# Kernel tuning notes

Measured on AMD Instinct MI355X. Metric: run time of the kernel, lower is better.

Reference implementation:

```python
import jax, jax.numpy as jnp
import numpy as np

N, F, D, K, H, O = 100000, 128, 16, 8, 256, 256  # nodes, feat, degree, num_hash, hash_dim, out_dim


def setup_inputs() -> dict:
    key = jax.random.key(0)
    k1, k2, k3, k4, k5 = jax.random.split(key, 5)
    x = jax.random.normal(k1, (N, F), dtype=jnp.float32)
    nbr_idx = jax.random.randint(k2, (N, D), 0, N, dtype=jnp.int32)
    # fixed sign hash matrices, one per hasher: {+1,-1}^{F x H}
    R = (jax.random.uniform(k3, (K, F, H)) > 0.5).astype(jnp.float32) * 2.0 - 1.0
    lim = float(np.sqrt(6.0 / (K * H + O)))  # xavier_uniform for Linear(K*H, O)
    Ws = jax.random.uniform(k4, (O, K * H), jnp.float32, -lim, lim)
    Wn = jax.random.uniform(k5, (O, K * H), jnp.float32, -lim, lim)
    bias = jnp.zeros((O,), dtype=jnp.float32)
    return {"x": x, "nbr_idx": nbr_idx, "R": R, "Ws": Ws, "Wn": Wn, "bias": bias}


def reference(x, nbr_idx, R, Ws, Wn, bias):
    n, f = x.shape
    k, _, h = R.shape
    # gather neighbor feats [N, D, F] and degree-mean -> [N, F]
    # (hashing is linear, so mean(hash(neigh)) == hash(mean(neigh)))
    neigh_mean = jnp.mean(x[nbr_idx], axis=1)
    # hash with all K hashers and concatenate streams: [N, K*H]
    hashed_neigh = jnp.einsum('nf,kfh->nkh', neigh_mean, R).reshape(n, k * h)
    hashed_self = jnp.einsum('nf,kfh->nkh', x, R).reshape(n, k * h)
    out = hashed_neigh @ Wn.T + hashed_self @ Ws.T + bias
    return jax.nn.elu(out)
```

## Files before the change

kernel.cpp:

```cpp
#include <hip/hip_runtime.h>
#include <hip/hip_bf16.h>
#include <math.h>

#define NN 100000
#define FF 128
#define DD 16
#define KK 8
#define HH 256
#define OO 256
#define KH 2048

using frag_t  = __attribute__((ext_vector_type(8))) short;
using f32x4   = __attribute__((ext_vector_type(4))) float;
using ushort8 = __attribute__((ext_vector_type(8))) unsigned short;

static __device__ __forceinline__ float bf2f(unsigned int u16) {
    union { unsigned int i; float f; } v; v.i = u16 << 16; return v.f;
}
static __device__ __forceinline__ unsigned short f2bf(float f) {
    union { float f; unsigned int i; } v; v.f = f;
    unsigned int x = v.i;
    x += 0x7fffu + ((x >> 16) & 1u);
    return (unsigned short)(x >> 16);
}

__global__ __launch_bounds__(256) void k_cast(const float* __restrict__ x,
                                              unsigned short* __restrict__ xb) {
    int t = blockIdx.x * 256 + threadIdx.x;
    const float4* xv = (const float4*)x;
    float4 a = xv[2 * t], b = xv[2 * t + 1];
    ushort8 o;
    o[0] = f2bf(a.x); o[1] = f2bf(a.y); o[2] = f2bf(a.z); o[3] = f2bf(a.w);
    o[4] = f2bf(b.x); o[5] = f2bf(b.y); o[6] = f2bf(b.z); o[7] = f2bf(b.w);
    *(ushort8*)(xb + (size_t)t * 8) = o;
}

__global__ __launch_bounds__(256) void k_wgemm(const float* __restrict__ R,
                                               const float* __restrict__ Ws,
                                               const float* __restrict__ Wn,
                                               float* __restrict__ P) {
    __shared__ float a_s[16][68];
    __shared__ float w_s[16][68];
    int bx = blockIdx.x, by = blockIdx.y, bz = blockIdx.z;
    const float* W = (bx < 2) ? Wn : Ws;
    int fbase = (bx & 1) * 64;
    int t = threadIdx.x;
    int tx = t & 15, ty = t >> 4;
    int lf = t >> 2;
    int j4 = (t & 3) * 4;
    float acc[4][4] = {};
    const float* Rb = R + (size_t)bz * (FF * HH) + (size_t)(fbase + lf) * HH;
    const float* Wb = W + (size_t)(by * 64 + lf) * KH + (size_t)bz * 256;
    for (int ks = 0; ks < 16; ++ks) {
        float4 av = *(const float4*)(Rb + ks * 16 + j4);
        float4 wv = *(const float4*)(Wb + ks * 16 + j4);
        __syncthreads();
        a_s[j4 + 0][lf] = av.x; a_s[j4 + 1][lf] = av.y;
        a_s[j4 + 2][lf] = av.z; a_s[j4 + 3][lf] = av.w;
        w_s[j4 + 0][lf] = wv.x; w_s[j4 + 1][lf] = wv.y;
        w_s[j4 + 2][lf] = wv.z; w_s[j4 + 3][lf] = wv.w;
        __syncthreads();
#pragma unroll
        for (int jj = 0; jj < 16; ++jj) {
            float ar[4], wr[4];
#pragma unroll
            for (int i = 0; i < 4; ++i) ar[i] = a_s[jj][ty * 4 + i];
#pragma unroll
            for (int j = 0; j < 4; ++j) wr[j] = w_s[jj][tx * 4 + j];
#pragma unroll
            for (int i = 0; i < 4; ++i)
#pragma unroll
                for (int j = 0; j < 4; ++j) acc[i][j] += ar[i] * wr[j];
        }
    }
    float* Pb = P + (size_t)bz * 65536 + (size_t)(bx * 64) * 256 + by * 64;
#pragma unroll
    for (int i = 0; i < 4; ++i) {
        float4 v = make_float4(acc[i][0], acc[i][1], acc[i][2], acc[i][3]);
        *(float4*)(Pb + (size_t)(ty * 4 + i) * 256 + tx * 4) = v;
    }
}

__global__ __launch_bounds__(256) void k_comb(const float* __restrict__ P,
                                              unsigned short* __restrict__ Bbf) {
    __shared__ float tsh[64][65];
    int bf = blockIdx.x, bo = blockIdx.y;
    int t = threadIdx.x;
    for (int e = t; e < 4096; e += 256) {
        int r = e >> 6, c = e & 63;
        float s = 0.f;
#pragma unroll
        for (int z = 0; z < 8; ++z)
            s += P[(size_t)z * 65536 + (size_t)(bf * 64 + r) * 256 + bo * 64 + c];
        tsh[r][c] = s;
    }
    __syncthreads();
    for (int e = t; e < 4096; e += 256) {
        int r = e >> 6, c = e & 63;
        Bbf[(size_t)(bo * 64 + r) * 256 + bf * 64 + c] = f2bf(tsh[c][r]);
    }
}

__global__ __launch_bounds__(512, 4) void k_fused(const unsigned short* __restrict__ xb,
                                                  const int* __restrict__ nbr,
                                                  const unsigned short* __restrict__ Bw,
                                                  const float* __restrict__ bias,
                                                  float* __restrict__ C) {
    __shared__ unsigned short Als[64][264];
    __shared__ unsigned short Bls[256][72];
    int m0 = blockIdx.x * 64;
    int t = threadIdx.x;
    int lane = t & 63, wv = t >> 6;
    int l15 = lane & 15, quad = lane >> 4;

    ushort8 bst[4];
    int brow[4], bcol[4];
#pragma unroll
    for (int s = 0; s < 4; ++s) {
        int c = s * 512 + t;
        brow[s] = c >> 3; bcol[s] = (c & 7) * 8;
        bst[s] = *(const ushort8*)(Bw + (size_t)brow[s] * 256 + bcol[s]);
    }

    const int rbase = wv * 8;
#pragma unroll 2
    for (int r = 0; r < 8; ++r) {
        int row = rbase + r;
        int node = m0 + row; if (node >= NN) node = NN - 1;
        node = __builtin_amdgcn_readfirstlane(node);
        const int* nb = nbr + (size_t)node * 16;
        unsigned int self = *(const unsigned int*)(xb + (size_t)node * 128 + lane * 2);
        float s0 = 0.f, s1 = 0.f;
#pragma unroll
        for (int d = 0; d < 16; ++d) {
            int idx = nb[d];
            unsigned int v = *(const unsigned int*)(xb + (size_t)idx * 128 + lane * 2);
            s0 += bf2f(v & 0xffffu);
            s1 += bf2f(v >> 16);
        }
        s0 *= 0.0625f; s1 *= 0.0625f;
        *(unsigned int*)&Als[row][lane * 2] =
            (unsigned int)f2bf(s0) | ((unsigned int)f2bf(s1) << 16);
        *(unsigned int*)&Als[row][128 + lane * 2] = self;
    }
#pragma unroll
    for (int s = 0; s < 4; ++s) *(ushort8*)&Bls[brow[s]][bcol[s]] = bst[s];
    __syncthreads();

    f32x4 acc[4][2] = {};
#pragma unroll 1
    for (int kt = 0; kt < 4; ++kt) {
        if (kt < 3) {
#pragma unroll
            for (int s = 0; s < 4; ++s)
                bst[s] = *(const ushort8*)(Bw + (size_t)brow[s] * 256 + (kt + 1) * 64 + bcol[s]);
        }
#pragma unroll
        for (int k2 = 0; k2 < 2; ++k2) {
            frag_t af[4], bfr[2];
#pragma unroll
            for (int i = 0; i < 4; ++i)
                af[i] = *(const frag_t*)&Als[i * 16 + l15][kt * 64 + k2 * 32 + quad * 8];
#pragma unroll
            for (int j = 0; j < 2; ++j)
                bfr[j] = *(const frag_t*)&Bls[wv * 32 + j * 16 + l15][k2 * 32 + quad * 8];
#pragma unroll
            for (int i = 0; i < 4; ++i)
#pragma unroll
                for (int j = 0; j < 2; ++j)
                    acc[i][j] = __builtin_amdgcn_mfma_f32_16x16x32_bf16(af[i], bfr[j], acc[i][j], 0, 0, 0);
        }
        __syncthreads();
        if (kt < 3) {
#pragma unroll
            for (int s = 0; s < 4; ++s) *(ushort8*)&Bls[brow[s]][bcol[s]] = bst[s];
            __syncthreads();
        }
    }
#pragma unroll
    for (int j = 0; j < 2; ++j) {
        int col = wv * 32 + j * 16 + l15;
        float bv = bias[col];
#pragma unroll
        for (int i = 0; i < 4; ++i) {
            int row0 = m0 + i * 16 + quad * 4;
#pragma unroll
            for (int r = 0; r < 4; ++r) {
                int row = row0 + r;
                if (row < NN) {
                    float v = acc[i][j][r] + bv;
                    C[(size_t)row * 256 + col] = (v > 0.f) ? v : expm1f(v);
                }
            }
        }
    }
}

extern "C" void kernel_launch(void* const* d_in, const int* in_sizes, int n_in,
                              void* d_out, int out_size, void* d_ws, size_t ws_size,
                              hipStream_t stream) {
    const float* x    = (const float*)d_in[0];
    const int*   nbr  = (const int*)d_in[1];
    const float* R    = (const float*)d_in[2];
    const float* Ws   = (const float*)d_in[3];
    const float* Wn   = (const float*)d_in[4];
    const float* bias = (const float*)d_in[5];
    float* out = (float*)d_out;

    char* ws = (char*)d_ws;
    unsigned short* xb  = (unsigned short*)(ws);
    float*          P   = (float*)(ws + 25600000);
    unsigned short* Bbf = (unsigned short*)(ws + 25600000 + 2097152);

    hipLaunchKernelGGL(k_cast,   dim3(6250),    dim3(256), 0, stream, x, xb);
    hipLaunchKernelGGL(k_wgemm,  dim3(4, 4, 8), dim3(256), 0, stream, R, Ws, Wn, P);
    hipLaunchKernelGGL(k_comb,   dim3(4, 4),    dim3(256), 0, stream, P, Bbf);
    hipLaunchKernelGGL(k_fused,  dim3(1563),    dim3(512), 0, stream, xb, nbr, Bbf, bias, out);
}
```

Measured before the change: 270.2 us.

## Widen neighbor gather, read B fragments from global, stage output stores

```diff
diff --git a/kernel.cpp b/kernel.cpp
--- a/kernel.cpp
+++ b/kernel.cpp
@@ -16,6 +16,12 @@
 
 static __device__ __forceinline__ float bf2f(unsigned int u16) {
     union { unsigned int i; float f; } v; v.i = u16 << 16; return v.f;
+}
+static __device__ __forceinline__ float blo(unsigned int u) {
+    union { unsigned int i; float f; } v; v.i = u << 16; return v.f;
+}
+static __device__ __forceinline__ float bhi(unsigned int u) {
+    union { unsigned int i; float f; } v; v.i = u & 0xffff0000u; return v.f;
 }
 static __device__ __forceinline__ unsigned short f2bf(float f) {
     union { float f; unsigned int i; } v; v.f = f;
@@ -106,92 +112,99 @@
                                                   const unsigned short* __restrict__ Bw,
                                                   const float* __restrict__ bias,
                                                   float* __restrict__ C) {
-    __shared__ unsigned short Als[64][264];
-    __shared__ unsigned short Bls[256][72];
+    __shared__ __align__(16) char smraw[64 * 264 * 2];
+    unsigned short (*Als)[264] = (unsigned short (*)[264])smraw;
+    float* Fls = (float*)smraw;
+    const int FLS_W = 260;
+
     int m0 = blockIdx.x * 64;
     int t = threadIdx.x;
     int lane = t & 63, wv = t >> 6;
     int l15 = lane & 15, quad = lane >> 4;
-
-    ushort8 bst[4];
-    int brow[4], bcol[4];
-#pragma unroll
-    for (int s = 0; s < 4; ++s) {
-        int c = s * 512 + t;
-        brow[s] = c >> 3; bcol[s] = (c & 7) * 8;
-        bst[s] = *(const ushort8*)(Bw + (size_t)brow[s] * 256 + bcol[s]);
-    }
-
-    const int rbase = wv * 8;
-#pragma unroll 2
-    for (int r = 0; r < 8; ++r) {
-        int row = rbase + r;
+    int l16 = lane & 15, r4 = lane >> 4;
+    int selbase = (lane & 48) << 2;
+
+#pragma unroll
+    for (int g = 0; g < 2; ++g) {
+        int row = wv * 8 + g * 4 + r4;
         int node = m0 + row; if (node >= NN) node = NN - 1;
-        node = __builtin_amdgcn_readfirstlane(node);
-        const int* nb = nbr + (size_t)node * 16;
-        unsigned int self = *(const unsigned int*)(xb + (size_t)node * 128 + lane * 2);
-        float s0 = 0.f, s1 = 0.f;
-#pragma unroll
-        for (int d = 0; d < 16; ++d) {
-            int idx = nb[d];
-            unsigned int v = *(const unsigned int*)(xb + (size_t)idx * 128 + lane * 2);
-            s0 += bf2f(v & 0xffffu);
-            s1 += bf2f(v >> 16);
-        }
-        s0 *= 0.0625f; s1 *= 0.0625f;
-        *(unsigned int*)&Als[row][lane * 2] =
-            (unsigned int)f2bf(s0) | ((unsigned int)f2bf(s1) << 16);
-        *(unsigned int*)&Als[row][128 + lane * 2] = self;
-    }
-#pragma unroll
-    for (int s = 0; s < 4; ++s) *(ushort8*)&Bls[brow[s]][bcol[s]] = bst[s];
+        int myidx = nbr[(size_t)node * 16 + l16];
+        uint4 selfv = *(const uint4*)(xb + (size_t)node * 128 + l16 * 8);
+        float s[8] = {0.f, 0.f, 0.f, 0.f, 0.f, 0.f, 0.f, 0.f};
+#pragma unroll
+        for (int h = 0; h < 2; ++h) {
+            uint4 gv[8];
+#pragma unroll
+            for (int d = 0; d < 8; ++d) {
+                int bi = __builtin_amdgcn_ds_bpermute(selbase + ((h * 8 + d) << 2), myidx);
+                gv[d] = *(const uint4*)(xb + (size_t)bi * 128 + l16 * 8);
+            }
+#pragma unroll
+            for (int d = 0; d < 8; ++d) {
+                s[0] += blo(gv[d].x); s[1] += bhi(gv[d].x);
+                s[2] += blo(gv[d].y); s[3] += bhi(gv[d].y);
+                s[4] += blo(gv[d].z); s[5] += bhi(gv[d].z);
+                s[6] += blo(gv[d].w); s[7] += bhi(gv[d].w);
+            }
+        }
+        ushort8 o;
+#pragma unroll
+        for (int k = 0; k < 8; ++k) o[k] = f2bf(s[k] * 0.0625f);
+        *(ushort8*)&Als[row][l16 * 8] = o;
+        *(uint4*)&Als[row][128 + l16 * 8] = selfv;
+    }
     __syncthreads();
 
     f32x4 acc[4][2] = {};
 #pragma unroll 1
     for (int kt = 0; kt < 4; ++kt) {
-        if (kt < 3) {
-#pragma unroll
-            for (int s = 0; s < 4; ++s)
-                bst[s] = *(const ushort8*)(Bw + (size_t)brow[s] * 256 + (kt + 1) * 64 + bcol[s]);
-        }
 #pragma unroll
         for (int k2 = 0; k2 < 2; ++k2) {
-            frag_t af[4], bfr[2];
+            frag_t bfr[2], af[4];
+#pragma unroll
+            for (int j = 0; j < 2; ++j)
+                bfr[j] = *(const frag_t*)(Bw + (size_t)(wv * 32 + j * 16 + l15) * 256
+                                             + kt * 64 + k2 * 32 + quad * 8);
 #pragma unroll
             for (int i = 0; i < 4; ++i)
                 af[i] = *(const frag_t*)&Als[i * 16 + l15][kt * 64 + k2 * 32 + quad * 8];
 #pragma unroll
-            for (int j = 0; j < 2; ++j)
-                bfr[j] = *(const frag_t*)&Bls[wv * 32 + j * 16 + l15][k2 * 32 + quad * 8];
-#pragma unroll
             for (int i = 0; i < 4; ++i)
 #pragma unroll
                 for (int j = 0; j < 2; ++j)
                     acc[i][j] = __builtin_amdgcn_mfma_f32_16x16x32_bf16(af[i], bfr[j], acc[i][j], 0, 0, 0);
         }
-        __syncthreads();
-        if (kt < 3) {
-#pragma unroll
-            for (int s = 0; s < 4; ++s) *(ushort8*)&Bls[brow[s]][bcol[s]] = bst[s];
-            __syncthreads();
-        }
-    }
-#pragma unroll
-    for (int j = 0; j < 2; ++j) {
-        int col = wv * 32 + j * 16 + l15;
-        float bv = bias[col];
-#pragma unroll
-        for (int i = 0; i < 4; ++i) {
-            int row0 = m0 + i * 16 + quad * 4;
-#pragma unroll
-            for (int r = 0; r < 4; ++r) {
-                int row = row0 + r;
-                if (row < NN) {
-                    float v = acc[i][j][r] + bv;
-                    C[(size_t)row * 256 + col] = (v > 0.f) ? v : expm1f(v);
+    }
+
+    float bv[2];
+#pragma unroll
+    for (int j = 0; j < 2; ++j) bv[j] = bias[wv * 32 + j * 16 + l15];
+#pragma unroll
+    for (int p = 0; p < 2; ++p) {
+        __syncthreads();
+#pragma unroll
+        for (int ii = 0; ii < 2; ++ii) {
+            int i = p * 2 + ii;
+#pragma unroll
+            for (int j = 0; j < 2; ++j) {
+                int col = wv * 32 + j * 16 + l15;
+#pragma unroll
+                for (int r = 0; r < 4; ++r) {
+                    int lr = ii * 16 + quad * 4 + r;
+                    float v = acc[i][j][r] + bv[j];
+                    v = (v > 0.f) ? v : expm1f(v);
+                    Fls[lr * FLS_W + col] = v;
                 }
             }
+        }
+        __syncthreads();
+#pragma unroll
+        for (int q = 0; q < 4; ++q) {
+            int f4 = q * 512 + t;
+            int lr = f4 >> 6, c4 = f4 & 63;
+            int grow = m0 + p * 32 + lr;
+            if (grow < NN)
+                *(float4*)(C + (size_t)grow * 256 + c4 * 4) = *(const float4*)&Fls[lr * FLS_W + c4 * 4];
         }
     }
 }
```

New measurement: 256.7 us. 1.05x faster.
